# Performance work log

Hardware: AMD Instinct MI355X
Metric: run time of the kernel (lower is better)

Reference implementation:

```python
import jax, jax.numpy as jnp
import numpy as np

B, S, H, E, V = 64, 256, 1024, 256, 32000

def setup_inputs() -> dict:
    key = jax.random.key(0)
    ks = jax.random.split(key, 16)
    sc = 0.02
    return {
        'x': jax.random.randint(ks[0], (B, 1), 0, V),
        'dec_hs': jax.random.normal(ks[1], (1, B, H), jnp.float32),
        'enc_output': jax.random.normal(ks[2], (S, B, H), jnp.float32),
        'emb_table': jax.random.normal(ks[3], (V, E), jnp.float32) * sc,
        'w1_W': jax.random.normal(ks[4], (H, H), jnp.float32) * sc,
        'w1_b': jnp.zeros((H,), jnp.float32),
        'w2_W': jax.random.normal(ks[5], (H, H), jnp.float32) * sc,
        'w2_b': jnp.zeros((H,), jnp.float32),
        'v_W': jax.random.normal(ks[6], (1, H), jnp.float32) * sc,
        'v_b': jnp.zeros((1,), jnp.float32),
        'gru_W_ih': jax.random.normal(ks[7], (3 * H, H + E), jnp.float32) * sc,
        'gru_W_hh': jax.random.normal(ks[8], (3 * H, H), jnp.float32) * sc,
        'gru_b_ih': jnp.zeros((3 * H,), jnp.float32),
        'gru_b_hh': jnp.zeros((3 * H,), jnp.float32),
        'fc_W': jax.random.normal(ks[9], (V, H), jnp.float32) * sc,
        'fc_b': jnp.zeros((V,), jnp.float32),
    }

def reference(x, dec_hs, enc_output, emb_table, w1_W, w1_b, w2_W, w2_b,
              v_W, v_b, gru_W_ih, gru_W_hh, gru_b_ih, gru_b_hh, fc_W, fc_b):
    # ---- Bahdanau additive attention ----
    dec = jnp.transpose(dec_hs, (1, 0, 2))        # [B,1,H]
    enc = jnp.transpose(enc_output, (1, 0, 2))    # [B,S,H]
    feat = jnp.tanh(dec @ w1_W.T + w1_b + enc @ w2_W.T + w2_b)  # [B,S,H]
    scores = feat @ v_W.T + v_b                   # [B,S,1]
    attn = jax.nn.softmax(scores, axis=1)         # [B,S,1]
    context = jnp.sum(attn * enc, axis=1)         # [B,H]
    # ---- embedding lookup + concat ----
    emb = emb_table[x[:, 0]]                      # [B,E]
    gru_in = jnp.concatenate([context, emb], axis=-1)  # [B,H+E]
    # ---- single-step GRU (PyTorch gate convention) ----
    h = dec_hs[0]                                 # [B,H]
    gi = gru_in @ gru_W_ih.T + gru_b_ih           # [B,3H]
    gh = h @ gru_W_hh.T + gru_b_hh                # [B,3H]
    gi_r, gi_z, gi_n = jnp.split(gi, 3, axis=-1)
    gh_r, gh_z, gh_n = jnp.split(gh, 3, axis=-1)
    r = jax.nn.sigmoid(gi_r + gh_r)
    z = jax.nn.sigmoid(gi_z + gh_z)
    n = jnp.tanh(gi_n + r * gh_n)
    h_new = (1.0 - z) * n + z * h                 # [B,H]
    # ---- output projection ----
    fc_out = h_new @ fc_W.T + fc_b                # [B,V]
    return fc_out, h_new[None], attn
```

## Files before the change

### kernel.cpp

```cpp
#include <hip/hip_runtime.h>

#define BB 64
#define SS 256
#define HH 1024
#define EE 256
#define VV 32000

typedef unsigned short u16;
typedef __attribute__((ext_vector_type(4))) unsigned short u16x4;
typedef __attribute__((ext_vector_type(8))) short s16x8;
typedef __attribute__((ext_vector_type(4))) float f32x4;

typedef const void __attribute__((address_space(1)))* gas_p;
typedef void __attribute__((address_space(3)))* las_p;

__device__ __forceinline__ u16 f2bf(float f) {
  unsigned u = __builtin_bit_cast(unsigned, f);
  u += 0x7fffu + ((u >> 16) & 1u);
  return (u16)(u >> 16);
}
__device__ __forceinline__ float bf2f(u16 u) {
  return __builtin_bit_cast(float, ((unsigned)u) << 16);
}
__device__ __forceinline__ void gload16(const void* g, void* l) {
  __builtin_amdgcn_global_load_lds((gas_p)g, (las_p)l, 16, 0, 0);
}
#define MFMA16(a, b, c) __builtin_amdgcn_mfma_f32_16x16x32_bf16(a, b, c, 0, 0, 0)

__global__ __launch_bounds__(256) void k_convert(const float* __restrict__ enc,
    const float* __restrict__ w2, const float* __restrict__ dec,
    u16* __restrict__ Ap, u16* __restrict__ w2b, u16* __restrict__ hb) {
  int bid = blockIdx.x, t = threadIdx.x;
  const float* src;
  u16* dst;
  if (bid < BB * SS) {
    int b = bid >> 8, s = bid & 255;
    src = enc + (size_t)(s * BB + b) * HH;
    dst = Ap + (size_t)bid * HH;
  } else if (bid < BB * SS + HH) {
    int r = bid - BB * SS;
    src = w2 + (size_t)r * HH;
    dst = w2b + (size_t)r * HH;
  } else {
    int b = bid - (BB * SS + HH);
    src = dec + (size_t)b * HH;
    dst = hb + (size_t)b * HH;
  }
  f32x4 v = *(const f32x4*)(src + t * 4);
  u16x4 o = { f2bf(v[0]), f2bf(v[1]), f2bf(v[2]), f2bf(v[3]) };
  *(u16x4*)(dst + t * 4) = o;
}

__global__ __launch_bounds__(256) void k_dbmm(const u16* __restrict__ hb,
    const float* __restrict__ w1, float* __restrict__ dbp) {
  int kc = blockIdx.y;
  int kb = kc * 128;
  int n0 = blockIdx.x * 128;
  __shared__ u16 Ws[2][128 * 32];
  int t = threadIdx.x, lane = t & 63, w = t >> 6;
  int wm = w >> 1, wn = w & 1, l15 = lane & 15, lg = lane >> 4;
  f32x4 acc[2][4] = {};
  int kx = (lg ^ ((l15 >> 1) & 3)) * 8;
  int wrow = t >> 1, wh = t & 1;
  int xr = (wrow >> 1) & 3;
  int s0 = (2 * wh) ^ xr, s1 = (2 * wh + 1) ^ xr;
  const float* gW = w1 + (size_t)(n0 + wrow) * HH + kb + wh * 16;
  const u16* gA = hb + kb + lg * 8;
  f32x4 c0 = *(const f32x4*)(gW);
  f32x4 c1 = *(const f32x4*)(gW + 4);
  f32x4 c2 = *(const f32x4*)(gW + 8);
  f32x4 c3 = *(const f32x4*)(gW + 12);
  s16x8 a0 = *(const s16x8*)(gA + (size_t)(wm * 32 + l15) * HH);
  s16x8 a1 = *(const s16x8*)(gA + (size_t)(wm * 32 + 16 + l15) * HH);
  {
    u16* lw = &Ws[0][wrow * 32];
    u16x4 o0 = { f2bf(c0[0]), f2bf(c0[1]), f2bf(c0[2]), f2bf(c0[3]) };
    u16x4 o1 = { f2bf(c1[0]), f2bf(c1[1]), f2bf(c1[2]), f2bf(c1[3]) };
    u16x4 o2 = { f2bf(c2[0]), f2bf(c2[1]), f2bf(c2[2]), f2bf(c2[3]) };
    u16x4 o3 = { f2bf(c3[0]), f2bf(c3[1]), f2bf(c3[2]), f2bf(c3[3]) };
    *(u16x4*)(lw + s0 * 8) = o0; *(u16x4*)(lw + s0 * 8 + 4) = o1;
    *(u16x4*)(lw + s1 * 8) = o2; *(u16x4*)(lw + s1 * 8 + 4) = o3;
  }
  __syncthreads();
  for (int it = 0; it < 4; ++it) {
    int nlast = (it < 3);
    f32x4 n0v, n1v, n2v, n3v;
    s16x8 an0, an1;
    if (nlast) {
      int k1 = (it + 1) * 32;
      n0v = *(const f32x4*)(gW + k1);
      n1v = *(const f32x4*)(gW + k1 + 4);
      n2v = *(const f32x4*)(gW + k1 + 8);
      n3v = *(const f32x4*)(gW + k1 + 12);
      an0 = *(const s16x8*)(gA + (size_t)(wm * 32 + l15) * HH + k1);
      an1 = *(const s16x8*)(gA + (size_t)(wm * 32 + 16 + l15) * HH + k1);
    }
    const u16* wb = Ws[it & 1];
    s16x8 bfr[4];
#pragma unroll
    for (int ni = 0; ni < 4; ++ni)
      bfr[ni] = *(const s16x8*)&wb[(wn * 64 + ni * 16 + l15) * 32 + kx];
#pragma unroll
    for (int ni = 0; ni < 4; ++ni) {
      acc[0][ni] = MFMA16(a0, bfr[ni], acc[0][ni]);
      acc[1][ni] = MFMA16(a1, bfr[ni], acc[1][ni]);
    }
    if (nlast) {
      u16* lw = &Ws[(it + 1) & 1][wrow * 32];
      u16x4 o0 = { f2bf(n0v[0]), f2bf(n0v[1]), f2bf(n0v[2]), f2bf(n0v[3]) };
      u16x4 o1 = { f2bf(n1v[0]), f2bf(n1v[1]), f2bf(n1v[2]), f2bf(n1v[3]) };
      u16x4 o2 = { f2bf(n2v[0]), f2bf(n2v[1]), f2bf(n2v[2]), f2bf(n2v[3]) };
      u16x4 o3 = { f2bf(n3v[0]), f2bf(n3v[1]), f2bf(n3v[2]), f2bf(n3v[3]) };
      *(u16x4*)(lw + s0 * 8) = o0; *(u16x4*)(lw + s0 * 8 + 4) = o1;
      *(u16x4*)(lw + s1 * 8) = o2; *(u16x4*)(lw + s1 * 8 + 4) = o3;
      a0 = an0; a1 = an1;
    }
    __syncthreads();
  }
  float* Pb = dbp + (size_t)kc * 64 * HH;
#pragma unroll
  for (int mi = 0; mi < 2; ++mi)
#pragma unroll
    for (int ni = 0; ni < 4; ++ni)
#pragma unroll
      for (int r = 0; r < 4; ++r) {
        int m = wm * 32 + mi * 16 + lg * 4 + r;
        int n = n0 + wn * 64 + ni * 16 + l15;
        Pb[(size_t)m * HH + n] = acc[mi][ni][r];
      }
}

__global__ __launch_bounds__(256) void k_biggemm(const u16* __restrict__ Ap,
    const u16* __restrict__ Bw, const float* __restrict__ w1b,
    const float* __restrict__ w2bias, const float* __restrict__ dbp,
    const float* __restrict__ vW, float* __restrict__ sp) {
  __shared__ u16 As[128 * 64];
  __shared__ u16 Bs[128 * 64];
  __shared__ float sc[2][128];
  int bid = blockIdx.x;
  int mt = ((bid >> 6) << 3) | (bid & 7);
  int nt = (bid >> 3) & 7;
  int t = threadIdx.x, lane = t & 63, w = t >> 6;
  int wm = w >> 1, wn = w & 1, l15 = lane & 15, lg = lane >> 4;
  int m0 = mt * 128, n0 = nt * 128;
  int b = m0 >> 8;
  f32x4 acc[4][4] = {};
  int srow = w * 32 + (lane >> 3);
  int cswz = ((lane & 7) ^ (lane >> 3)) * 8;
  const u16* gA = Ap + (size_t)(m0 + srow) * HH + cswz;
  const u16* gB = Bw + (size_t)(n0 + srow) * HH + cswz;
  u16* lA = As + w * 32 * 64;
  u16* lB = Bs + w * 32 * 64;
  for (int it = 0; it < 16; ++it) {
    int k0 = it * 64;
#pragma unroll
    for (int i = 0; i < 4; ++i)
      gload16(gA + (size_t)i * 8 * HH + k0, lA + i * 8 * 64);
#pragma unroll
    for (int i = 0; i < 4; ++i)
      gload16(gB + (size_t)i * 8 * HH + k0, lB + i * 8 * 64);
    __syncthreads();
#pragma unroll
    for (int kk = 0; kk < 2; ++kk) {
      s16x8 af[4], bfr[4];
#pragma unroll
      for (int mi = 0; mi < 4; ++mi) {
        int row = wm * 64 + mi * 16 + l15;
        int slot = (kk * 4 + lg) ^ (row & 7);
        af[mi] = *(const s16x8*)&As[row * 64 + slot * 8];
      }
#pragma unroll
      for (int ni = 0; ni < 4; ++ni) {
        int row = wn * 64 + ni * 16 + l15;
        int slot = (kk * 4 + lg) ^ (row & 7);
        bfr[ni] = *(const s16x8*)&Bs[row * 64 + slot * 8];
      }
#pragma unroll
      for (int mi = 0; mi < 4; ++mi)
#pragma unroll
        for (int ni = 0; ni < 4; ++ni)
          acc[mi][ni] = MFMA16(af[mi], bfr[ni], acc[mi][ni]);
    }
    __syncthreads();
  }
  const float* vv = vW + n0;
  float dbs[4];
#pragma unroll
  for (int ni = 0; ni < 4; ++ni) {
    int nl = wn * 64 + ni * 16 + l15;
    int n = n0 + nl;
    float s = w1b[n] + w2bias[n];
#pragma unroll
    for (int p = 0; p < 8; ++p) s += dbp[(size_t)p * 64 * HH + (size_t)b * HH + n];
    dbs[ni] = s;
  }
#pragma unroll
  for (int mi = 0; mi < 4; ++mi) {
#pragma unroll
    for (int r = 0; r < 4; ++r) {
      float p = 0.f;
#pragma unroll
      for (int ni = 0; ni < 4; ++ni) {
        int nl = wn * 64 + ni * 16 + l15;
        p += tanhf(acc[mi][ni][r] + dbs[ni]) * vv[nl];
      }
      p += __shfl_xor(p, 1); p += __shfl_xor(p, 2);
      p += __shfl_xor(p, 4); p += __shfl_xor(p, 8);
      if (l15 == 0) sc[wn][wm * 64 + mi * 16 + lg * 4 + r] = p;
    }
  }
  __syncthreads();
  if (t < 128) sp[(size_t)(m0 + t) * 8 + nt] = sc[0][t] + sc[1][t];
}

__global__ __launch_bounds__(256) void k_ctxsm(const float* __restrict__ sp,
    const float* __restrict__ vb, const u16* __restrict__ Ap,
    float* __restrict__ attn, float* __restrict__ ctxp) {
  int sc = blockIdx.x, b = blockIdx.y, t = threadIdx.x;
  int lane = t & 63, w = t >> 6;
  const float* row = sp + (size_t)(b * SS + t) * 8;
  f32x4 a = *(const f32x4*)row;
  f32x4 c = *(const f32x4*)(row + 4);
  float score = a[0] + a[1] + a[2] + a[3] + c[0] + c[1] + c[2] + c[3] + vb[0];
  __shared__ float rmax[4], rsum[4], at[SS];
  float m = score;
  for (int mk = 1; mk < 64; mk <<= 1) m = fmaxf(m, __shfl_xor(m, mk));
  if (lane == 0) rmax[w] = m;
  __syncthreads();
  m = fmaxf(fmaxf(rmax[0], rmax[1]), fmaxf(rmax[2], rmax[3]));
  float e = expf(score - m);
  float ssum = e;
  for (int mk = 1; mk < 64; mk <<= 1) ssum += __shfl_xor(ssum, mk);
  if (lane == 0) rsum[w] = ssum;
  __syncthreads();
  float tot = rsum[0] + rsum[1] + rsum[2] + rsum[3];
  float av = e / tot;
  at[t] = av;
  if (sc == 0) attn[(size_t)b * SS + t] = av;
  __syncthreads();
  const u16* base = Ap + (size_t)(b * SS + sc * 32) * HH + t * 4;
  float a0 = 0.f, a1 = 0.f, a2 = 0.f, a3 = 0.f;
#pragma unroll 4
  for (int s = 0; s < 32; ++s) {
    u16x4 v = *(const u16x4*)(base + (size_t)s * HH);
    float w_ = at[sc * 32 + s];
    a0 += w_ * bf2f(v[0]); a1 += w_ * bf2f(v[1]);
    a2 += w_ * bf2f(v[2]); a3 += w_ * bf2f(v[3]);
  }
  f32x4 o = { a0, a1, a2, a3 };
  *(f32x4*)&ctxp[(size_t)(b * 8 + sc) * HH + t * 4] = o;
}

__global__ __launch_bounds__(256) void k_ctxcomb(const float* __restrict__ ctxp,
    const int* __restrict__ x, const float* __restrict__ emb,
    u16* __restrict__ gin) {
  int b = blockIdx.x, t = threadIdx.x;
  f32x4 s = {0.f, 0.f, 0.f, 0.f};
#pragma unroll
  for (int p = 0; p < 8; ++p)
    s += *(const f32x4*)&ctxp[(size_t)(b * 8 + p) * HH + t * 4];
  u16x4 o = { f2bf(s[0]), f2bf(s[1]), f2bf(s[2]), f2bf(s[3]) };
  *(u16x4*)(gin + (size_t)b * 1280 + t * 4) = o;
  int xb = x[b];
  gin[(size_t)b * 1280 + HH + t] = f2bf(emb[(size_t)xb * EE + t]);
}

__global__ __launch_bounds__(256) void k_gru(const u16* __restrict__ gin,
    const u16* __restrict__ hb, const float* __restrict__ Wih,
    const float* __restrict__ Whh, float* __restrict__ P) {
  int y = blockIdx.y;
  int z = (y >= 5);
  const u16* Ab = z ? hb : gin;
  const float* Wf = z ? Whh : Wih;
  int K = z ? HH : (HH + EE);
  int kb = (z ? (y - 5) : y) * 256;
  int n0 = blockIdx.x * 128;
  __shared__ u16 Ws[2][128 * 32];
  int t = threadIdx.x, lane = t & 63, w = t >> 6;
  int wm = w >> 1, wn = w & 1, l15 = lane & 15, lg = lane >> 4;
  f32x4 acc[2][4] = {};
  int kx = (lg ^ ((l15 >> 1) & 3)) * 8;
  int wrow = t >> 1, wh = t & 1;
  int xr = (wrow >> 1) & 3;
  int s0 = (2 * wh) ^ xr, s1 = (2 * wh + 1) ^ xr;
  const float* gW = Wf + (size_t)(n0 + wrow) * K + kb + wh * 16;
  const u16* gA = Ab + kb + lg * 8;
  f32x4 c0 = *(const f32x4*)(gW);
  f32x4 c1 = *(const f32x4*)(gW + 4);
  f32x4 c2 = *(const f32x4*)(gW + 8);
  f32x4 c3 = *(const f32x4*)(gW + 12);
  s16x8 a0 = *(const s16x8*)(gA + (size_t)(wm * 32 + l15) * K);
  s16x8 a1 = *(const s16x8*)(gA + (size_t)(wm * 32 + 16 + l15) * K);
  {
    u16* lw = &Ws[0][wrow * 32];
    u16x4 o0 = { f2bf(c0[0]), f2bf(c0[1]), f2bf(c0[2]), f2bf(c0[3]) };
    u16x4 o1 = { f2bf(c1[0]), f2bf(c1[1]), f2bf(c1[2]), f2bf(c1[3]) };
    u16x4 o2 = { f2bf(c2[0]), f2bf(c2[1]), f2bf(c2[2]), f2bf(c2[3]) };
    u16x4 o3 = { f2bf(c3[0]), f2bf(c3[1]), f2bf(c3[2]), f2bf(c3[3]) };
    *(u16x4*)(lw + s0 * 8) = o0; *(u16x4*)(lw + s0 * 8 + 4) = o1;
    *(u16x4*)(lw + s1 * 8) = o2; *(u16x4*)(lw + s1 * 8 + 4) = o3;
  }
  __syncthreads();
  for (int it = 0; it < 8; ++it) {
    int nlast = (it < 7);
    f32x4 n0v, n1v, n2v, n3v;
    s16x8 an0, an1;
    if (nlast) {
      int k1 = (it + 1) * 32;
      n0v = *(const f32x4*)(gW + k1);
      n1v = *(const f32x4*)(gW + k1 + 4);
      n2v = *(const f32x4*)(gW + k1 + 8);
      n3v = *(const f32x4*)(gW + k1 + 12);
      an0 = *(const s16x8*)(gA + (size_t)(wm * 32 + l15) * K + k1);
      an1 = *(const s16x8*)(gA + (size_t)(wm * 32 + 16 + l15) * K + k1);
    }
    const u16* wb = Ws[it & 1];
    s16x8 bfr[4];
#pragma unroll
    for (int ni = 0; ni < 4; ++ni)
      bfr[ni] = *(const s16x8*)&wb[(wn * 64 + ni * 16 + l15) * 32 + kx];
#pragma unroll
    for (int ni = 0; ni < 4; ++ni) {
      acc[0][ni] = MFMA16(a0, bfr[ni], acc[0][ni]);
      acc[1][ni] = MFMA16(a1, bfr[ni], acc[1][ni]);
    }
    if (nlast) {
      u16* lw = &Ws[(it + 1) & 1][wrow * 32];
      u16x4 o0 = { f2bf(n0v[0]), f2bf(n0v[1]), f2bf(n0v[2]), f2bf(n0v[3]) };
      u16x4 o1 = { f2bf(n1v[0]), f2bf(n1v[1]), f2bf(n1v[2]), f2bf(n1v[3]) };
      u16x4 o2 = { f2bf(n2v[0]), f2bf(n2v[1]), f2bf(n2v[2]), f2bf(n2v[3]) };
      u16x4 o3 = { f2bf(n3v[0]), f2bf(n3v[1]), f2bf(n3v[2]), f2bf(n3v[3]) };
      *(u16x4*)(lw + s0 * 8) = o0; *(u16x4*)(lw + s0 * 8 + 4) = o1;
      *(u16x4*)(lw + s1 * 8) = o2; *(u16x4*)(lw + s1 * 8 + 4) = o3;
      a0 = an0; a1 = an1;
    }
    __syncthreads();
  }
  float* Pb = P + (size_t)y * 64 * 3072;
#pragma unroll
  for (int mi = 0; mi < 2; ++mi)
#pragma unroll
    for (int ni = 0; ni < 4; ++ni)
#pragma unroll
      for (int r = 0; r < 4; ++r) {
        int m = wm * 32 + mi * 16 + lg * 4 + r;
        int n = n0 + wn * 64 + ni * 16 + l15;
        Pb[(size_t)m * 3072 + n] = acc[mi][ni][r];
      }
}

__global__ __launch_bounds__(256) void k_gates(const float* __restrict__ P,
    const float* __restrict__ bih, const float* __restrict__ bhh,
    const float* __restrict__ dec, float* __restrict__ hn_out,
    u16* __restrict__ hnb) {
  int b = blockIdx.x, t = threadIdx.x;
#pragma unroll
  for (int j = 0; j < 4; ++j) {
    int h = t + j * 256;
    float gir = 0.f, giz = 0.f, gin_ = 0.f, ghr = 0.f, ghz = 0.f, ghn = 0.f;
#pragma unroll
    for (int y = 0; y < 5; ++y) {
      const float* r = P + (size_t)(y * 64 + b) * 3072;
      gir += r[h]; giz += r[h + 1024]; gin_ += r[h + 2048];
    }
#pragma unroll
    for (int y = 0; y < 4; ++y) {
      const float* r = P + (size_t)((5 + y) * 64 + b) * 3072;
      ghr += r[h]; ghz += r[h + 1024]; ghn += r[h + 2048];
    }
    float rr = 1.f / (1.f + expf(-(gir + bih[h] + ghr + bhh[h])));
    float zz = 1.f / (1.f + expf(-(giz + bih[1024 + h] + ghz + bhh[1024 + h])));
    float nn = tanhf(gin_ + bih[2048 + h] + rr * (ghn + bhh[2048 + h]));
    float hv = dec[(size_t)b * HH + h];
    float hnew = (1.f - zz) * nn + zz * hv;
    hn_out[(size_t)b * HH + h] = hnew;
    hnb[(size_t)b * HH + h] = f2bf(hnew);
  }
}

__global__ __launch_bounds__(256) void k_fc(const u16* __restrict__ hnb,
    const float* __restrict__ W, const float* __restrict__ bias,
    float* __restrict__ out) {
  int n0 = blockIdx.x * 64;
  __shared__ u16 Ws[2][64 * 32];
  int t = threadIdx.x, lane = t & 63, w = t >> 6;
  int wm = w >> 1, wn = w & 1, l15 = lane & 15, lg = lane >> 4;
  f32x4 acc[2][2] = {};
  int kx = (lg ^ ((l15 >> 1) & 3)) * 8;
  int wrow = t >> 2;
  int sq = ((t & 3) ^ ((t >> 3) & 3)) * 8;
  const float* gW = W + (size_t)(n0 + wrow) * HH + (t & 3) * 8;
  const u16* gA = hnb + lg * 8;
  f32x4 c0 = *(const f32x4*)(gW);
  f32x4 c1 = *(const f32x4*)(gW + 4);
  s16x8 a0 = *(const s16x8*)(gA + (size_t)(wm * 32 + l15) * HH);
  s16x8 a1 = *(const s16x8*)(gA + (size_t)(wm * 32 + 16 + l15) * HH);
  {
    u16* lw = &Ws[0][wrow * 32 + sq];
    u16x4 o0 = { f2bf(c0[0]), f2bf(c0[1]), f2bf(c0[2]), f2bf(c0[3]) };
    u16x4 o1 = { f2bf(c1[0]), f2bf(c1[1]), f2bf(c1[2]), f2bf(c1[3]) };
    *(u16x4*)(lw) = o0; *(u16x4*)(lw + 4) = o1;
  }
  __syncthreads();
  for (int it = 0; it < 32; ++it) {
    int nlast = (it < 31);
    f32x4 n0v, n1v;
    s16x8 an0, an1;
    if (nlast) {
      int k1 = (it + 1) * 32;
      n0v = *(const f32x4*)(gW + k1);
      n1v = *(const f32x4*)(gW + k1 + 4);
      an0 = *(const s16x8*)(gA + (size_t)(wm * 32 + l15) * HH + k1);
      an1 = *(const s16x8*)(gA + (size_t)(wm * 32 + 16 + l15) * HH + k1);
    }
    const u16* wb = Ws[it & 1];
    s16x8 bfr[2];
#pragma unroll
    for (int ni = 0; ni < 2; ++ni)
      bfr[ni] = *(const s16x8*)&wb[(wn * 32 + ni * 16 + l15) * 32 + kx];
#pragma unroll
    for (int ni = 0; ni < 2; ++ni) {
      acc[0][ni] = MFMA16(a0, bfr[ni], acc[0][ni]);
      acc[1][ni] = MFMA16(a1, bfr[ni], acc[1][ni]);
    }
    if (nlast) {
      u16* lw = &Ws[(it + 1) & 1][wrow * 32 + sq];
      u16x4 o0 = { f2bf(n0v[0]), f2bf(n0v[1]), f2bf(n0v[2]), f2bf(n0v[3]) };
      u16x4 o1 = { f2bf(n1v[0]), f2bf(n1v[1]), f2bf(n1v[2]), f2bf(n1v[3]) };
      *(u16x4*)(lw) = o0; *(u16x4*)(lw + 4) = o1;
      a0 = an0; a1 = an1;
    }
    __syncthreads();
  }
#pragma unroll
  for (int mi = 0; mi < 2; ++mi)
#pragma unroll
    for (int ni = 0; ni < 2; ++ni)
#pragma unroll
      for (int r = 0; r < 4; ++r) {
        int m = wm * 32 + mi * 16 + lg * 4 + r;
        int n = n0 + wn * 32 + ni * 16 + l15;
        out[(size_t)m * VV + n] = acc[mi][ni][r] + bias[n];
      }
}

extern "C" void kernel_launch(void* const* d_in, const int* in_sizes, int n_in,
                              void* d_out, int out_size, void* d_ws, size_t ws_size,
                              hipStream_t stream) {
  const int*   x      = (const int*)   d_in[0];
  const float* dec    = (const float*) d_in[1];
  const float* enc    = (const float*) d_in[2];
  const float* emb    = (const float*) d_in[3];
  const float* w1     = (const float*) d_in[4];
  const float* w1b    = (const float*) d_in[5];
  const float* w2     = (const float*) d_in[6];
  const float* w2bias = (const float*) d_in[7];
  const float* vW     = (const float*) d_in[8];
  const float* vb     = (const float*) d_in[9];
  const float* Wih    = (const float*) d_in[10];
  const float* Whh    = (const float*) d_in[11];
  const float* bih    = (const float*) d_in[12];
  const float* bhh    = (const float*) d_in[13];
  const float* fcW    = (const float*) d_in[14];
  const float* fcb    = (const float*) d_in[15];
  float* out = (float*)d_out;
  char* ws = (char*)d_ws;
  u16*   Ap    = (u16*)(ws);
  u16*   w2b   = (u16*)(ws + 33554432);
  u16*   hb    = (u16*)(ws + 35651584);
  u16*   gin   = (u16*)(ws + 35782656);
  u16*   hnb   = (u16*)(ws + 35946496);
  float* sp    = (float*)(ws + 36339712);
  float* P     = (float*)(ws + 36864000);
  float* dbp   = P;
  float* ctxp  = P + 524288;
  float* hn   = out + 2048000;
  float* attn = out + 2113536;

  k_convert<<<BB * SS + HH + BB, 256, 0, stream>>>(enc, w2, dec, Ap, w2b, hb);
  k_dbmm<<<dim3(8, 8), 256, 0, stream>>>(hb, w1, dbp);
  k_biggemm<<<1024, 256, 0, stream>>>(Ap, w2b, w1b, w2bias, dbp, vW, sp);
  k_ctxsm<<<dim3(8, BB), 256, 0, stream>>>(sp, vb, Ap, attn, ctxp);
  k_ctxcomb<<<BB, 256, 0, stream>>>(ctxp, x, emb, gin);
  k_gru<<<dim3(24, 9), 256, 0, stream>>>(gin, hb, Wih, Whh, P);
  k_gates<<<BB, 256, 0, stream>>>(P, bih, bhh, dec, hn, hnb);
  k_fc<<<500, 256, 0, stream>>>(hnb, fcW, fcb, out);
}
```

Baseline: 145.9 us.

## Fuse enc fp32-to-bf16 conversion into attention GEMM and merge dbmm with convert

Drops the separate pass that converts enc_output (64 MB fp32) into a bf16 transposed copy. The big attention GEMM now loads fp32 enc rows directly, converts them in registers and writes them swizzled into LDS, prefetching the next K slice into registers. The context kernel reads fp32 enc directly. The small dec@W1 GEMM is merged with the W2/dec conversion into a single launch and converts dec on the fly. This removes a 64 MB read plus 32 MB write and a round trip, but the GEMM's A loads become strided fp32 register loads instead of async LDS loads, and the context pass reads twice as many bytes.

```diff
diff --git a/kernel.cpp b/kernel.cpp
--- a/kernel.cpp
+++ b/kernel.cpp
@@ -22,42 +22,45 @@
 __device__ __forceinline__ float bf2f(u16 u) {
   return __builtin_bit_cast(float, ((unsigned)u) << 16);
 }
+__device__ __forceinline__ s16x8 cvt8(f32x4 a, f32x4 b) {
+  s16x8 r;
+  r[0] = (short)f2bf(a[0]); r[1] = (short)f2bf(a[1]);
+  r[2] = (short)f2bf(a[2]); r[3] = (short)f2bf(a[3]);
+  r[4] = (short)f2bf(b[0]); r[5] = (short)f2bf(b[1]);
+  r[6] = (short)f2bf(b[2]); r[7] = (short)f2bf(b[3]);
+  return r;
+}
 __device__ __forceinline__ void gload16(const void* g, void* l) {
   __builtin_amdgcn_global_load_lds((gas_p)g, (las_p)l, 16, 0, 0);
 }
 #define MFMA16(a, b, c) __builtin_amdgcn_mfma_f32_16x16x32_bf16(a, b, c, 0, 0, 0)
 
-__global__ __launch_bounds__(256) void k_convert(const float* __restrict__ enc,
-    const float* __restrict__ w2, const float* __restrict__ dec,
-    u16* __restrict__ Ap, u16* __restrict__ w2b, u16* __restrict__ hb) {
+__global__ __launch_bounds__(256) void k_convdb(const float* __restrict__ w2,
+    const float* __restrict__ dec, const float* __restrict__ w1,
+    u16* __restrict__ w2b, u16* __restrict__ hb, float* __restrict__ dbp) {
+  __shared__ u16 Ws[2][128 * 32];
   int bid = blockIdx.x, t = threadIdx.x;
-  const float* src;
-  u16* dst;
-  if (bid < BB * SS) {
-    int b = bid >> 8, s = bid & 255;
-    src = enc + (size_t)(s * BB + b) * HH;
-    dst = Ap + (size_t)bid * HH;
-  } else if (bid < BB * SS + HH) {
-    int r = bid - BB * SS;
-    src = w2 + (size_t)r * HH;
-    dst = w2b + (size_t)r * HH;
-  } else {
-    int b = bid - (BB * SS + HH);
-    src = dec + (size_t)b * HH;
-    dst = hb + (size_t)b * HH;
-  }
-  f32x4 v = *(const f32x4*)(src + t * 4);
-  u16x4 o = { f2bf(v[0]), f2bf(v[1]), f2bf(v[2]), f2bf(v[3]) };
-  *(u16x4*)(dst + t * 4) = o;
-}
-
-__global__ __launch_bounds__(256) void k_dbmm(const u16* __restrict__ hb,
-    const float* __restrict__ w1, float* __restrict__ dbp) {
-  int kc = blockIdx.y;
+  if (bid < HH + BB) {
+    const float* src;
+    u16* dst;
+    if (bid < HH) {
+      src = w2 + (size_t)bid * HH;
+      dst = w2b + (size_t)bid * HH;
+    } else {
+      int b = bid - HH;
+      src = dec + (size_t)b * HH;
+      dst = hb + (size_t)b * HH;
+    }
+    f32x4 v = *(const f32x4*)(src + t * 4);
+    u16x4 o = { f2bf(v[0]), f2bf(v[1]), f2bf(v[2]), f2bf(v[3]) };
+    *(u16x4*)(dst + t * 4) = o;
+    return;
+  }
+  int bid2 = bid - (HH + BB);
+  int nt = bid2 & 7, kc = bid2 >> 3;
   int kb = kc * 128;
-  int n0 = blockIdx.x * 128;
-  __shared__ u16 Ws[2][128 * 32];
-  int t = threadIdx.x, lane = t & 63, w = t >> 6;
+  int n0 = nt * 128;
+  int lane = t & 63, w = t >> 6;
   int wm = w >> 1, wn = w & 1, l15 = lane & 15, lg = lane >> 4;
   f32x4 acc[2][4] = {};
   int kx = (lg ^ ((l15 >> 1) & 3)) * 8;
@@ -65,13 +68,15 @@
   int xr = (wrow >> 1) & 3;
   int s0 = (2 * wh) ^ xr, s1 = (2 * wh + 1) ^ xr;
   const float* gW = w1 + (size_t)(n0 + wrow) * HH + kb + wh * 16;
-  const u16* gA = hb + kb + lg * 8;
+  const float* dA = dec + kb + lg * 8;
   f32x4 c0 = *(const f32x4*)(gW);
   f32x4 c1 = *(const f32x4*)(gW + 4);
   f32x4 c2 = *(const f32x4*)(gW + 8);
   f32x4 c3 = *(const f32x4*)(gW + 12);
-  s16x8 a0 = *(const s16x8*)(gA + (size_t)(wm * 32 + l15) * HH);
-  s16x8 a1 = *(const s16x8*)(gA + (size_t)(wm * 32 + 16 + l15) * HH);
+  const float* r0 = dA + (size_t)(wm * 32 + l15) * HH;
+  const float* r1 = dA + (size_t)(wm * 32 + 16 + l15) * HH;
+  s16x8 a0 = cvt8(*(const f32x4*)r0, *(const f32x4*)(r0 + 4));
+  s16x8 a1 = cvt8(*(const f32x4*)r1, *(const f32x4*)(r1 + 4));
   {
     u16* lw = &Ws[0][wrow * 32];
     u16x4 o0 = { f2bf(c0[0]), f2bf(c0[1]), f2bf(c0[2]), f2bf(c0[3]) };
@@ -92,8 +97,8 @@
       n1v = *(const f32x4*)(gW + k1 + 4);
       n2v = *(const f32x4*)(gW + k1 + 8);
       n3v = *(const f32x4*)(gW + k1 + 12);
-      an0 = *(const s16x8*)(gA + (size_t)(wm * 32 + l15) * HH + k1);
-      an1 = *(const s16x8*)(gA + (size_t)(wm * 32 + 16 + l15) * HH + k1);
+      an0 = cvt8(*(const f32x4*)(r0 + k1), *(const f32x4*)(r0 + k1 + 4));
+      an1 = cvt8(*(const f32x4*)(r1 + k1), *(const f32x4*)(r1 + k1 + 4));
     }
     const u16* wb = Ws[it & 1];
     s16x8 bfr[4];
@@ -130,7 +135,7 @@
       }
 }
 
-__global__ __launch_bounds__(256) void k_biggemm(const u16* __restrict__ Ap,
+__global__ __launch_bounds__(256) void k_biggemm(const float* __restrict__ enc,
     const u16* __restrict__ Bw, const float* __restrict__ w1b,
     const float* __restrict__ w2bias, const float* __restrict__ dbp,
     const float* __restrict__ vW, float* __restrict__ sp) {
@@ -143,23 +148,42 @@
   int t = threadIdx.x, lane = t & 63, w = t >> 6;
   int wm = w >> 1, wn = w & 1, l15 = lane & 15, lg = lane >> 4;
   int m0 = mt * 128, n0 = nt * 128;
-  int b = m0 >> 8;
+  int b = mt >> 1;
+  int s0 = (mt & 1) * 128;
   f32x4 acc[4][4] = {};
   int srow = w * 32 + (lane >> 3);
   int cswz = ((lane & 7) ^ (lane >> 3)) * 8;
-  const u16* gA = Ap + (size_t)(m0 + srow) * HH + cswz;
   const u16* gB = Bw + (size_t)(n0 + srow) * HH + cswz;
-  u16* lA = As + w * 32 * 64;
   u16* lB = Bs + w * 32 * 64;
+  int ar = t & 127, aseg = t >> 7;
+  const float* gArow = enc + ((size_t)(s0 + ar) * BB + b) * HH + aseg * 32;
+  u16* aws = As + ar * 64;
+  int aswz[4];
+#pragma unroll
+  for (int j = 0; j < 4; ++j) aswz[j] = ((aseg * 4 + j) ^ (ar & 7)) * 8;
+  f32x4 ar_[8];
+#pragma unroll
+  for (int j = 0; j < 8; ++j) ar_[j] = *(const f32x4*)(gArow + j * 4);
   for (int it = 0; it < 16; ++it) {
     int k0 = it * 64;
 #pragma unroll
-    for (int i = 0; i < 4; ++i)
-      gload16(gA + (size_t)i * 8 * HH + k0, lA + i * 8 * 64);
+    for (int j = 0; j < 4; ++j) {
+      u16x4 lo = { f2bf(ar_[2 * j][0]), f2bf(ar_[2 * j][1]),
+                   f2bf(ar_[2 * j][2]), f2bf(ar_[2 * j][3]) };
+      u16x4 hi = { f2bf(ar_[2 * j + 1][0]), f2bf(ar_[2 * j + 1][1]),
+                   f2bf(ar_[2 * j + 1][2]), f2bf(ar_[2 * j + 1][3]) };
+      *(u16x4*)(aws + aswz[j]) = lo;
+      *(u16x4*)(aws + aswz[j] + 4) = hi;
+    }
 #pragma unroll
     for (int i = 0; i < 4; ++i)
       gload16(gB + (size_t)i * 8 * HH + k0, lB + i * 8 * 64);
     __syncthreads();
+    if (it < 15) {
+#pragma unroll
+      for (int j = 0; j < 8; ++j)
+        ar_[j] = *(const f32x4*)(gArow + k0 + 64 + j * 4);
+    }
 #pragma unroll
     for (int kk = 0; kk < 2; ++kk) {
       s16x8 af[4], bfr[4];
@@ -214,7 +238,7 @@
 }
 
 __global__ __launch_bounds__(256) void k_ctxsm(const float* __restrict__ sp,
-    const float* __restrict__ vb, const u16* __restrict__ Ap,
+    const float* __restrict__ vb, const float* __restrict__ enc,
     float* __restrict__ attn, float* __restrict__ ctxp) {
   int sc = blockIdx.x, b = blockIdx.y, t = threadIdx.x;
   int lane = t & 63, w = t >> 6;
@@ -238,14 +262,14 @@
   at[t] = av;
   if (sc == 0) attn[(size_t)b * SS + t] = av;
   __syncthreads();
-  const u16* base = Ap + (size_t)(b * SS + sc * 32) * HH + t * 4;
+  const float* base = enc + ((size_t)(sc * 32) * BB + b) * HH + t * 4;
   float a0 = 0.f, a1 = 0.f, a2 = 0.f, a3 = 0.f;
 #pragma unroll 4
   for (int s = 0; s < 32; ++s) {
-    u16x4 v = *(const u16x4*)(base + (size_t)s * HH);
+    f32x4 v = *(const f32x4*)(base + (size_t)s * BB * HH);
     float w_ = at[sc * 32 + s];
-    a0 += w_ * bf2f(v[0]); a1 += w_ * bf2f(v[1]);
-    a2 += w_ * bf2f(v[2]); a3 += w_ * bf2f(v[3]);
+    a0 += w_ * v[0]; a1 += w_ * v[1];
+    a2 += w_ * v[2]; a3 += w_ * v[3];
   }
   f32x4 o = { a0, a1, a2, a3 };
   *(f32x4*)&ctxp[(size_t)(b * 8 + sc) * HH + t * 4] = o;
@@ -465,22 +489,20 @@
   const float* fcb    = (const float*) d_in[15];
   float* out = (float*)d_out;
   char* ws = (char*)d_ws;
-  u16*   Ap    = (u16*)(ws);
-  u16*   w2b   = (u16*)(ws + 33554432);
-  u16*   hb    = (u16*)(ws + 35651584);
-  u16*   gin   = (u16*)(ws + 35782656);
-  u16*   hnb   = (u16*)(ws + 35946496);
-  float* sp    = (float*)(ws + 36339712);
-  float* P     = (float*)(ws + 36864000);
+  u16*   w2b   = (u16*)(ws);
+  u16*   hb    = (u16*)(ws + 2097152);
+  u16*   gin   = (u16*)(ws + 2228224);
+  u16*   hnb   = (u16*)(ws + 2392064);
+  float* sp    = (float*)(ws + 2523136);
+  float* P     = (float*)(ws + 3047424);
   float* dbp   = P;
   float* ctxp  = P + 524288;
   float* hn   = out + 2048000;
   float* attn = out + 2113536;
 
-  k_convert<<<BB * SS + HH + BB, 256, 0, stream>>>(enc, w2, dec, Ap, w2b, hb);
-  k_dbmm<<<dim3(8, 8), 256, 0, stream>>>(hb, w1, dbp);
-  k_biggemm<<<1024, 256, 0, stream>>>(Ap, w2b, w1b, w2bias, dbp, vW, sp);
-  k_ctxsm<<<dim3(8, BB), 256, 0, stream>>>(sp, vb, Ap, attn, ctxp);
+  k_convdb<<<HH + BB + 64, 256, 0, stream>>>(w2, dec, w1, w2b, hb, dbp);
+  k_biggemm<<<1024, 256, 0, stream>>>(enc, w2b, w1b, w2bias, dbp, vW, sp);
+  k_ctxsm<<<dim3(8, BB), 256, 0, stream>>>(sp, vb, enc, attn, ctxp);
   k_ctxcomb<<<BB, 256, 0, stream>>>(ctxp, x, emb, gin);
   k_gru<<<dim3(24, 9), 256, 0, stream>>>(gin, hb, Wih, Whh, P);
   k_gates<<<BB, 256, 0, stream>>>(P, bih, bhh, dec, hn, hnb);
```

New measurement: 180.4 us. +23.6%, slower.
